# Kernel optimization log

Hardware: AMD Instinct MI355X
Metric: run time of the kernel (lower is better)

## Reference

```python
import jax, jax.numpy as jnp
import numpy as np

INPUT_DIM = 1024
OUTPUT_DIM = 1024
SPLINE_POINTS = 4

def setup_inputs() -> dict:
    key = jax.random.key(0)
    k1, k2 = jax.random.split(key)
    x = jax.random.normal(k1, (4096, INPUT_DIM), dtype=jnp.float32)
    spline_coeffs = jax.random.normal(k2, (OUTPUT_DIM, INPUT_DIM, SPLINE_POINTS, 4), dtype=jnp.float32)
    return {"x": x, "spline_coeffs": spline_coeffs}

def reference(x, spline_coeffs):
    # Per-feature min-max normalization over the batch dim (as in the torch code,
    # where x[:, j].min()/max() are taken over the batch).
    xmin = jnp.min(x, axis=0, keepdims=True)   # [1, D]
    xmax = jnp.max(x, axis=0, keepdims=True)
    xn = (x - xmin) / (xmax - xmin)            # [B, D]

    # The original sums the cubic polynomial over all spline_points, so the
    # effective coefficients are the sum over the spline_points axis.
    c = jnp.sum(spline_coeffs, axis=2)         # [O, D, 4]

    x2 = xn * xn
    x3 = x2 * xn
    # out[b, o] = sum_d c0*x^3 + c1*x^2 + c2*x + c3
    out = (jnp.einsum('bd,od->bo', x3, c[..., 0])
           + jnp.einsum('bd,od->bo', x2, c[..., 1])
           + jnp.einsum('bd,od->bo', xn, c[..., 2])
           + jnp.sum(c[..., 3], axis=1)[None, :])
    return out
```

## Files before the change

### kernel.cpp

```cpp
#include <hip/hip_runtime.h>
#include <hip/hip_bf16.h>
#include <stdint.h>
#include <stddef.h>

typedef __bf16 bf16;
typedef __attribute__((ext_vector_type(4))) __bf16 bf16x4;
typedef __attribute__((ext_vector_type(8))) __bf16 bf16x8;
typedef __attribute__((ext_vector_type(4))) float f32x4;

#define BATCH 4096
#define DIM 1024
#define ODIM 1024
#define K3 3072

#define WS_CB     0
#define WS_BIAS   6291456
#define WS_PMIN   6295552
#define WS_PMAX   7344128
#define WS_MINV   8392704
#define WS_SCALE  8396800

#define ASYNC16(g, l)                                                          \
  __builtin_amdgcn_global_load_lds(                                            \
      (__attribute__((address_space(1))) void*)(g),                            \
      (__attribute__((address_space(3))) void*)(l), 16, 0, 0)

#define BARRIER()                     \
  do {                                \
    asm volatile("" ::: "memory");    \
    __builtin_amdgcn_s_barrier();     \
    asm volatile("" ::: "memory");    \
  } while (0)
#define WAIT_VM0() __builtin_amdgcn_s_waitcnt(0x0F00 | 0x0070)
#define WAIT_LGKM() __builtin_amdgcn_s_waitcnt(0xC07F)

__global__ void k_stream(const float* __restrict__ x,
                         float* __restrict__ pmin,
                         float* __restrict__ pmax,
                         const float* __restrict__ sp,
                         bf16* __restrict__ CB,
                         float* __restrict__ bias) {
  __shared__ float red[4];
  const int t = threadIdx.x;
  if (blockIdx.x < 256) {
    const int ch = blockIdx.x;
    const float* p = x + (size_t)ch * 16 * DIM + (t << 2);
    f32x4 mn = {1e30f, 1e30f, 1e30f, 1e30f};
    f32x4 mx = {-1e30f, -1e30f, -1e30f, -1e30f};
#pragma unroll
    for (int r = 0; r < 16; ++r) {
      f32x4 v = *(const f32x4*)(p + (size_t)r * DIM);
#pragma unroll
      for (int j = 0; j < 4; ++j) {
        mn[j] = fminf(mn[j], v[j]);
        mx[j] = fmaxf(mx[j], v[j]);
      }
    }
    *(f32x4*)(pmin + ch * DIM + (t << 2)) = mn;
    *(f32x4*)(pmax + ch * DIM + (t << 2)) = mx;
  } else {
    const int o = blockIdx.x - 256;
    const int d = t << 2;
    f32x4 s[4];
#pragma unroll
    for (int dd = 0; dd < 4; ++dd) {
      const float* p = sp + ((size_t)o * DIM + d + dd) * 16;
      f32x4 acc = *(const f32x4*)(p);
      acc += *(const f32x4*)(p + 4);
      acc += *(const f32x4*)(p + 8);
      acc += *(const f32x4*)(p + 12);
      s[dd] = acc;
    }
    size_t cb = (size_t)o * K3 + d;
    bf16x4 c0 = {(bf16)s[0][0], (bf16)s[1][0], (bf16)s[2][0], (bf16)s[3][0]};
    bf16x4 c1 = {(bf16)s[0][1], (bf16)s[1][1], (bf16)s[2][1], (bf16)s[3][1]};
    bf16x4 c2 = {(bf16)s[0][2], (bf16)s[1][2], (bf16)s[2][2], (bf16)s[3][2]};
    *(bf16x4*)(CB + cb) = c0;
    *(bf16x4*)(CB + cb + 1024) = c1;
    *(bf16x4*)(CB + cb + 2048) = c2;
    float v = s[0][3] + s[1][3] + s[2][3] + s[3][3];
#pragma unroll
    for (int off = 32; off > 0; off >>= 1) v += __shfl_down(v, off, 64);
    int lane = t & 63, w = t >> 6;
    if (lane == 0) red[w] = v;
    __syncthreads();
    if (t == 0) bias[o] = red[0] + red[1] + red[2] + red[3];
  }
}

__global__ void k_minmax_final(const float* __restrict__ pmin,
                               const float* __restrict__ pmax,
                               float* __restrict__ minv,
                               float* __restrict__ scale) {
  __shared__ float smn[4][64], smx[4][64];
  const int t = threadIdx.x;
  const int lane = t & 63;
  const int w = t >> 6;
  const int col = blockIdx.x * 64 + lane;
  float mn = 1e30f, mx = -1e30f;
#pragma unroll 8
  for (int ch = w; ch < 256; ch += 4) {
    mn = fminf(mn, pmin[ch * DIM + col]);
    mx = fmaxf(mx, pmax[ch * DIM + col]);
  }
  smn[w][lane] = mn;
  smx[w][lane] = mx;
  __syncthreads();
  if (w == 0) {
    mn = fminf(fminf(smn[0][lane], smn[1][lane]), fminf(smn[2][lane], smn[3][lane]));
    mx = fmaxf(fmaxf(smx[0][lane], smx[1][lane]), fmaxf(smx[2][lane], smx[3][lane]));
    minv[col] = mn;
    scale[col] = 1.0f / (mx - mn);
  }
}

#define MSOFF 98304
#define ABUF(b) ((b) * 24576)
#define BBUF(b) (49152 + (b) * 24576)
__global__ __launch_bounds__(512, 2) void k_gemm(const float* __restrict__ x,
                                                 const float* __restrict__ minv,
                                                 const float* __restrict__ scale,
                                                 const bf16* __restrict__ CBm,
                                                 const float* __restrict__ bias,
                                                 float* __restrict__ out) {
  __shared__ __attribute__((aligned(16))) char smem[106496];

  const int tid = threadIdx.x;
  const int wave = tid >> 6;
  const int lane = tid & 63;

  const int f = blockIdx.x;
  const int chunk = f & 7;
  const int idx = f >> 3;
  const int mt = ((chunk >> 1) << 3) + (idx >> 2);
  const int nt = ((chunk & 1) << 2) + (idx & 3);
  const int bm = mt * 128;
  const int bn = nt * 128;

  const int wr = (wave >> 2) * 64;
  const int wc = (wave & 3) * 32;
  const int mrow = lane & 15;
  const int kq = lane >> 4;

  const int prow = tid >> 2;
  const int u = tid & 3;
  const int aslot = (u ^ ((prow >> 1) & 3)) << 4;
  const float* xg = x + (size_t)(bm + prow) * DIM + u * 8;

  const char* gBp = (const char*)CBm + (size_t)(bn + (tid >> 2)) * 6144 +
                    (size_t)(((tid & 3) ^ ((tid >> 3) & 3)) << 4);

  if (tid < 256) {
    f32x4 m = *(const f32x4*)(minv + tid * 4);
    *(f32x4*)(smem + MSOFF + tid * 16) = m;
  } else {
    f32x4 s = *(const f32x4*)(scale + (tid - 256) * 4);
    *(f32x4*)(smem + MSOFF + 4096 + (tid - 256) * 16) = s;
  }

  f32x4 xa, xb;
#define LOADX(dtv)                                                            \
  do {                                                                        \
    xa = *(const f32x4*)(xg + (dtv) * 32);                                    \
    xb = *(const f32x4*)(xg + (dtv) * 32 + 4);                                \
  } while (0)

#define STAGE_B(buf, dtv)                                                     \
  do {                                                                        \
    const char* gb_ = gBp + (size_t)(dtv) * 64;                               \
    char* lb_ = smem + BBUF(buf) + wave * 1024;                               \
    ASYNC16(gb_, lb_);                                                        \
    ASYNC16(gb_ + 2048, lb_ + 8192);                                          \
    ASYNC16(gb_ + 4096, lb_ + 16384);                                         \
  } while (0)

#define POWERS_WRITE(abuf, dtv)                                               \
  do {                                                                        \
    const char* msp = smem + MSOFF + ((dtv) * 32 + u * 8) * 4;                \
    f32x4 mn0 = *(const f32x4*)(msp);                                         \
    f32x4 mn1 = *(const f32x4*)(msp + 16);                                    \
    f32x4 sc0 = *(const f32x4*)(msp + 4096);                                  \
    f32x4 sc1 = *(const f32x4*)(msp + 4112);                                  \
    f32x4 n0 = (xa - mn0) * sc0, n1 = (xb - mn1) * sc1;                       \
    f32x4 q0 = n0 * n0, q1 = n1 * n1;                                         \
    f32x4 c0v = q0 * n0, c1v = q1 * n1;                                       \
    bf16x8 w1, w2, w3;                                                        \
    _Pragma("unroll") for (int e = 0; e < 4; ++e) {                           \
      w3[e] = (bf16)c0v[e]; w3[e + 4] = (bf16)c1v[e];                         \
      w2[e] = (bf16)q0[e];  w2[e + 4] = (bf16)q1[e];                          \
      w1[e] = (bf16)n0[e];  w1[e + 4] = (bf16)n1[e];                          \
    }                                                                         \
    char* aw_ = smem + ABUF(abuf) + prow * 64 + aslot;                        \
    *(bf16x8*)(aw_) = w3;                                   \
    *(bf16x8*)(aw_ + 8192) = w2;                            \
    *(bf16x8*)(aw_ + 16384) = w1;                           \
  } while (0)

  f32x4 acc[4][2] = {};

#define COMPUTE(buf)                                                          \
  do {                                                                        \
    const char* ab_ = smem + ABUF(buf);                                       \
    const char* bb_ = smem + BBUF(buf);                                       \
    _Pragma("unroll") for (int p = 0; p < 3; ++p) {                           \
      bf16x8 bg[2];                                                           \
      _Pragma("unroll") for (int j = 0; j < 2; ++j) {                         \
        int rowb = wc + j * 16 + mrow;                                        \
        bg[j] = *(const bf16x8*)(bb_ + p * 8192 + rowb * 64 +                 \
                                 ((kq ^ ((rowb >> 1) & 3)) << 4));            \
      }                                                                       \
      bf16x8 af[4];                                                           \
      _Pragma("unroll") for (int i = 0; i < 4; ++i) {                         \
        int rowa = wr + i * 16 + mrow;                                        \
        af[i] = *(const bf16x8*)(ab_ + p * 8192 + rowa * 64 +                 \
                                 ((kq ^ ((rowa >> 1) & 3)) << 4));            \
      }                                                                       \
      _Pragma("unroll") for (int i = 0; i < 4; ++i)                           \
          _Pragma("unroll") for (int j = 0; j < 2; ++j)                       \
              acc[i][j] = __builtin_amdgcn_mfma_f32_16x16x32_bf16(            \
                  af[i], bg[j], acc[i][j], 0, 0, 0);                          \
    }                                                                         \
  } while (0)

  STAGE_B(0, 0);
  LOADX(0);
  WAIT_VM0();
  WAIT_LGKM();
  BARRIER();
  POWERS_WRITE(0, 0);
  LOADX(1);
  WAIT_LGKM();
  BARRIER();

#pragma unroll 2
  for (int dt = 0; dt < 32; ++dt) {
    if (dt < 31) STAGE_B((dt + 1) & 1, dt + 1);
    COMPUTE(dt & 1);
    if (dt < 31) POWERS_WRITE((dt + 1) & 1, dt + 1);
    WAIT_VM0();
    if (dt < 30) LOADX(dt + 2);
    WAIT_LGKM();
    BARRIER();
  }

  const int ccol = lane & 15;
  const int crow = (lane >> 4) * 4;
#pragma unroll
  for (int j = 0; j < 2; ++j) {
    const int col = bn + wc + j * 16 + ccol;
    const float bv = bias[col];
#pragma unroll
    for (int i = 0; i < 4; ++i) {
      const int row0 = bm + wr + i * 16 + crow;
#pragma unroll
      for (int r = 0; r < 4; ++r)
        out[(size_t)(row0 + r) * ODIM + col] = acc[i][j][r] + bv;
    }
  }
#undef LOADX
#undef STAGE_B
#undef POWERS_WRITE
#undef COMPUTE
}

extern "C" void kernel_launch(void* const* d_in, const int* in_sizes, int n_in,
                              void* d_out, int out_size, void* d_ws, size_t ws_size,
                              hipStream_t stream) {
  (void)in_sizes; (void)n_in; (void)out_size; (void)ws_size;
  const float* x = (const float*)d_in[0];
  const float* sp = (const float*)d_in[1];
  float* out = (float*)d_out;
  char* ws = (char*)d_ws;

  bf16* CBm = (bf16*)(ws + WS_CB);
  float* bias = (float*)(ws + WS_BIAS);
  float* pmin = (float*)(ws + WS_PMIN);
  float* pmax = (float*)(ws + WS_PMAX);
  float* minv = (float*)(ws + WS_MINV);
  float* scale = (float*)(ws + WS_SCALE);

  k_stream<<<1280, 256, 0, stream>>>(x, pmin, pmax, sp, CBm, bias);
  k_minmax_final<<<16, 256, 0, stream>>>(pmin, pmax, minv, scale);
  k_gemm<<<256, 512, 0, stream>>>(x, minv, scale, CBm, bias, out);
}
```

Before: 151.1 us.

## Warp-specialize GEMM into producer/consumer waves and fuse min/max via atomics

Per-feature min/max is now reduced with order-preserving integer atomicMin in the stream kernel, which removes the second reduction kernel and its partial-min/max buffers (a memset is added instead). The GEMM is split into four producer waves and four consumer waves. Producers load x, compute the normalized powers and stage B asynchronously, while consumers only run MFMAs, each now owning a 64x64 output tile. This is meant to overlap the power computation with matrix math and drop one launch, at the cost of only half the waves doing MFMA work and atomic contention on the min/max arrays.

```diff
diff --git a/kernel.cpp b/kernel.cpp
--- a/kernel.cpp
+++ b/kernel.cpp
@@ -15,10 +15,8 @@
 
 #define WS_CB     0
 #define WS_BIAS   6291456
-#define WS_PMIN   6295552
-#define WS_PMAX   7344128
-#define WS_MINV   8392704
-#define WS_SCALE  8396800
+#define WS_UMIN   6295552
+#define WS_UMAXC  6299648
 
 #define ASYNC16(g, l)                                                          \
   __builtin_amdgcn_global_load_lds(                                            \
@@ -31,12 +29,21 @@
     __builtin_amdgcn_s_barrier();     \
     asm volatile("" ::: "memory");    \
   } while (0)
+#define WAIT_VM(n) __builtin_amdgcn_s_waitcnt(0x0F00 | 0x0070 | ((n)&15) | ((((n)>>4)&3)<<14))
 #define WAIT_VM0() __builtin_amdgcn_s_waitcnt(0x0F00 | 0x0070)
 #define WAIT_LGKM() __builtin_amdgcn_s_waitcnt(0xC07F)
 
+__device__ __forceinline__ uint32_t enc_f32(float f) {
+  uint32_t u = __float_as_uint(f);
+  return (u & 0x80000000u) ? ~u : (u | 0x80000000u);
+}
+__device__ __forceinline__ float dec_f32(uint32_t k) {
+  return __uint_as_float((k & 0x80000000u) ? (k ^ 0x80000000u) : ~k);
+}
+
 __global__ void k_stream(const float* __restrict__ x,
-                         float* __restrict__ pmin,
-                         float* __restrict__ pmax,
+                         uint32_t* __restrict__ umin,
+                         uint32_t* __restrict__ umaxc,
                          const float* __restrict__ sp,
                          bf16* __restrict__ CB,
                          float* __restrict__ bias) {
@@ -56,8 +63,12 @@
         mx[j] = fmaxf(mx[j], v[j]);
       }
     }
-    *(f32x4*)(pmin + ch * DIM + (t << 2)) = mn;
-    *(f32x4*)(pmax + ch * DIM + (t << 2)) = mx;
+    const int c = t << 2;
+#pragma unroll
+    for (int j = 0; j < 4; ++j) {
+      atomicMin(&umin[c + j], enc_f32(mn[j]));
+      atomicMin(&umaxc[c + j], ~enc_f32(mx[j]));
+    }
   } else {
     const int o = blockIdx.x - 256;
     const int d = t << 2;
@@ -88,38 +99,12 @@
   }
 }
 
-__global__ void k_minmax_final(const float* __restrict__ pmin,
-                               const float* __restrict__ pmax,
-                               float* __restrict__ minv,
-                               float* __restrict__ scale) {
-  __shared__ float smn[4][64], smx[4][64];
-  const int t = threadIdx.x;
-  const int lane = t & 63;
-  const int w = t >> 6;
-  const int col = blockIdx.x * 64 + lane;
-  float mn = 1e30f, mx = -1e30f;
-#pragma unroll 8
-  for (int ch = w; ch < 256; ch += 4) {
-    mn = fminf(mn, pmin[ch * DIM + col]);
-    mx = fmaxf(mx, pmax[ch * DIM + col]);
-  }
-  smn[w][lane] = mn;
-  smx[w][lane] = mx;
-  __syncthreads();
-  if (w == 0) {
-    mn = fminf(fminf(smn[0][lane], smn[1][lane]), fminf(smn[2][lane], smn[3][lane]));
-    mx = fmaxf(fmaxf(smx[0][lane], smx[1][lane]), fmaxf(smx[2][lane], smx[3][lane]));
-    minv[col] = mn;
-    scale[col] = 1.0f / (mx - mn);
-  }
-}
-
 #define MSOFF 98304
 #define ABUF(b) ((b) * 24576)
 #define BBUF(b) (49152 + (b) * 24576)
 __global__ __launch_bounds__(512, 2) void k_gemm(const float* __restrict__ x,
-                                                 const float* __restrict__ minv,
-                                                 const float* __restrict__ scale,
+                                                 const uint32_t* __restrict__ umin,
+                                                 const uint32_t* __restrict__ umaxc,
                                                  const bf16* __restrict__ CBm,
                                                  const float* __restrict__ bias,
                                                  float* __restrict__ out) {
@@ -137,129 +122,182 @@
   const int bm = mt * 128;
   const int bn = nt * 128;
 
-  const int wr = (wave >> 2) * 64;
-  const int wc = (wave & 3) * 32;
+  const int wr = ((wave & 3) >> 1) * 64;
+  const int wc = (wave & 1) * 64;
   const int mrow = lane & 15;
   const int kq = lane >> 4;
 
-  const int prow = tid >> 2;
-  const int u = tid & 3;
-  const int aslot = (u ^ ((prow >> 1) & 3)) << 4;
-  const float* xg = x + (size_t)(bm + prow) * DIM + u * 8;
-
-  const char* gBp = (const char*)CBm + (size_t)(bn + (tid >> 2)) * 6144 +
-                    (size_t)(((tid & 3) ^ ((tid >> 3) & 3)) << 4);
-
-  if (tid < 256) {
-    f32x4 m = *(const f32x4*)(minv + tid * 4);
-    *(f32x4*)(smem + MSOFF + tid * 16) = m;
-  } else {
-    f32x4 s = *(const f32x4*)(scale + (tid - 256) * 4);
-    *(f32x4*)(smem + MSOFF + 4096 + (tid - 256) * 16) = s;
-  }
-
-  f32x4 xa, xb;
-#define LOADX(dtv)                                                            \
+  const int ptid = (tid >= 256) ? (tid - 256) : 0;
+  const int pr = ptid >> 1;
+  const int h = tid & 1;
+  const int sA0 = ((h * 2 + 0) ^ ((pr >> 1) & 3)) << 4;
+  const int sA1 = ((h * 2 + 1) ^ ((pr >> 1) & 3)) << 4;
+  const float* xg = x + (size_t)(bm + pr) * DIM + h * 16;
+
+  const char* gB[6];
+  int ldsBoff[6];
+  if (wave >= 4) {
+    const int pk = wave - 4;
+#pragma unroll
+    for (int i = 0; i < 6; ++i) {
+      int L = (pk * 6 + i) * 1024 + lane * 16;
+      int p_ = L >> 13;
+      int rem = L & 8191;
+      int row_ = rem >> 6;
+      int u_ = (rem >> 4) & 3;
+      int us = u_ ^ ((row_ >> 1) & 3);
+      gB[i] = (const char*)CBm + (size_t)(bn + row_) * 6144 + p_ * 2048 + us * 16;
+      ldsBoff[i] = (pk * 6 + i) * 1024;
+    }
+  }
+
+  f32x4 xA0, xA1, xA2, xA3, xB0, xB1, xB2, xB3;
+#define LOADX(S, dtv)                                                         \
   do {                                                                        \
-    xa = *(const f32x4*)(xg + (dtv) * 32);                                    \
-    xb = *(const f32x4*)(xg + (dtv) * 32 + 4);                                \
+    const float* xp_ = xg + (dtv) * 32;                                       \
+    S##0 = *(const f32x4*)(xp_);                                              \
+    S##1 = *(const f32x4*)(xp_ + 4);                                          \
+    S##2 = *(const f32x4*)(xp_ + 8);                                          \
+    S##3 = *(const f32x4*)(xp_ + 12);                                         \
   } while (0)
 
 #define STAGE_B(buf, dtv)                                                     \
   do {                                                                        \
-    const char* gb_ = gBp + (size_t)(dtv) * 64;                               \
-    char* lb_ = smem + BBUF(buf) + wave * 1024;                               \
-    ASYNC16(gb_, lb_);                                                        \
-    ASYNC16(gb_ + 2048, lb_ + 8192);                                          \
-    ASYNC16(gb_ + 4096, lb_ + 16384);                                         \
-  } while (0)
-
-#define POWERS_WRITE(abuf, dtv)                                               \
+    _Pragma("unroll") for (int i_ = 0; i_ < 6; ++i_)                          \
+        ASYNC16(gB[i_] + (size_t)(dtv) * 64,                                  \
+                smem + BBUF(buf) + ldsBoff[i_]);                              \
+  } while (0)
+
+#define PK8(lo, hi, dst)                                                      \
+  _Pragma("unroll") for (int e_ = 0; e_ < 4; ++e_) {                          \
+    dst[e_] = (bf16)lo[e_];                                                   \
+    dst[e_ + 4] = (bf16)hi[e_];                                               \
+  }
+
+#define POWERS(buf, dtv, S)                                                   \
   do {                                                                        \
-    const char* msp = smem + MSOFF + ((dtv) * 32 + u * 8) * 4;                \
-    f32x4 mn0 = *(const f32x4*)(msp);                                         \
-    f32x4 mn1 = *(const f32x4*)(msp + 16);                                    \
-    f32x4 sc0 = *(const f32x4*)(msp + 4096);                                  \
-    f32x4 sc1 = *(const f32x4*)(msp + 4112);                                  \
-    f32x4 n0 = (xa - mn0) * sc0, n1 = (xb - mn1) * sc1;                       \
-    f32x4 q0 = n0 * n0, q1 = n1 * n1;                                         \
-    f32x4 c0v = q0 * n0, c1v = q1 * n1;                                       \
-    bf16x8 w1, w2, w3;                                                        \
-    _Pragma("unroll") for (int e = 0; e < 4; ++e) {                           \
-      w3[e] = (bf16)c0v[e]; w3[e + 4] = (bf16)c1v[e];                         \
-      w2[e] = (bf16)q0[e];  w2[e + 4] = (bf16)q1[e];                          \
-      w1[e] = (bf16)n0[e];  w1[e + 4] = (bf16)n1[e];                          \
-    }                                                                         \
-    char* aw_ = smem + ABUF(abuf) + prow * 64 + aslot;                        \
-    *(bf16x8*)(aw_) = w3;                                   \
-    *(bf16x8*)(aw_ + 8192) = w2;                            \
-    *(bf16x8*)(aw_ + 16384) = w1;                           \
-  } while (0)
-
-  f32x4 acc[4][2] = {};
+    const char* msp = smem + MSOFF + ((dtv) * 32 + h * 16) * 4;               \
+    f32x4 n0 = (S##0 - *(const f32x4*)(msp)) * *(const f32x4*)(msp + 4096);   \
+    f32x4 n1 = (S##1 - *(const f32x4*)(msp + 16)) * *(const f32x4*)(msp + 4112); \
+    f32x4 n2 = (S##2 - *(const f32x4*)(msp + 32)) * *(const f32x4*)(msp + 4128); \
+    f32x4 n3 = (S##3 - *(const f32x4*)(msp + 48)) * *(const f32x4*)(msp + 4144); \
+    f32x4 q0 = n0 * n0, q1 = n1 * n1, q2 = n2 * n2, q3 = n3 * n3;             \
+    f32x4 c0 = q0 * n0, c1 = q1 * n1, c2 = q2 * n2, c3 = q3 * n3;             \
+    bf16x8 w3a, w3b, w2a, w2b, w1a, w1b;                                      \
+    PK8(c0, c1, w3a) PK8(c2, c3, w3b)                                         \
+    PK8(q0, q1, w2a) PK8(q2, q3, w2b)                                         \
+    PK8(n0, n1, w1a) PK8(n2, n3, w1b)                                         \
+    char* aw_ = smem + ABUF(buf) + pr * 64;                                   \
+    *(bf16x8*)(aw_ + sA0) = w3a;                                              \
+    *(bf16x8*)(aw_ + sA1) = w3b;                                              \
+    *(bf16x8*)(aw_ + 8192 + sA0) = w2a;                                       \
+    *(bf16x8*)(aw_ + 8192 + sA1) = w2b;                                       \
+    *(bf16x8*)(aw_ + 16384 + sA0) = w1a;                                      \
+    *(bf16x8*)(aw_ + 16384 + sA1) = w1b;                                      \
+  } while (0)
+
+  f32x4 acc[4][4] = {};
 
 #define COMPUTE(buf)                                                          \
   do {                                                                        \
     const char* ab_ = smem + ABUF(buf);                                       \
     const char* bb_ = smem + BBUF(buf);                                       \
     _Pragma("unroll") for (int p = 0; p < 3; ++p) {                           \
-      bf16x8 bg[2];                                                           \
-      _Pragma("unroll") for (int j = 0; j < 2; ++j) {                         \
-        int rowb = wc + j * 16 + mrow;                                        \
-        bg[j] = *(const bf16x8*)(bb_ + p * 8192 + rowb * 64 +                 \
-                                 ((kq ^ ((rowb >> 1) & 3)) << 4));            \
-      }                                                                       \
-      bf16x8 af[4];                                                           \
+      bf16x8 af[4], bg[4];                                                    \
       _Pragma("unroll") for (int i = 0; i < 4; ++i) {                         \
         int rowa = wr + i * 16 + mrow;                                        \
         af[i] = *(const bf16x8*)(ab_ + p * 8192 + rowa * 64 +                 \
                                  ((kq ^ ((rowa >> 1) & 3)) << 4));            \
+        int rowb = wc + i * 16 + mrow;                                        \
+        bg[i] = *(const bf16x8*)(bb_ + p * 8192 + rowb * 64 +                 \
+                                 ((kq ^ ((rowb >> 1) & 3)) << 4));            \
       }                                                                       \
       _Pragma("unroll") for (int i = 0; i < 4; ++i)                           \
-          _Pragma("unroll") for (int j = 0; j < 2; ++j)                       \
+          _Pragma("unroll") for (int j = 0; j < 4; ++j)                       \
               acc[i][j] = __builtin_amdgcn_mfma_f32_16x16x32_bf16(            \
                   af[i], bg[j], acc[i][j], 0, 0, 0);                          \
     }                                                                         \
   } while (0)
 
-  STAGE_B(0, 0);
-  LOADX(0);
-  WAIT_VM0();
-  WAIT_LGKM();
+  if (wave >= 4) {
+    const int c = (tid - 256) << 2;
+    f32x4 mnv, scv;
+#pragma unroll
+    for (int j = 0; j < 4; ++j) {
+      float mnf = dec_f32(umin[c + j]);
+      float mxf = dec_f32(~umaxc[c + j]);
+      mnv[j] = mnf;
+      scv[j] = 1.0f / (mxf - mnf);
+    }
+    *(f32x4*)(smem + MSOFF + c * 4) = mnv;
+    *(f32x4*)(smem + MSOFF + 4096 + c * 4) = scv;
+    STAGE_B(0, 0);
+    LOADX(xA, 0);
+    WAIT_VM0();
+    WAIT_LGKM();
+  }
   BARRIER();
-  POWERS_WRITE(0, 0);
-  LOADX(1);
-  WAIT_LGKM();
+  if (wave >= 4) {
+    POWERS(0, 0, xA);
+    LOADX(xB, 1);
+    WAIT_LGKM();
+  }
   BARRIER();
 
-#pragma unroll 2
-  for (int dt = 0; dt < 32; ++dt) {
-    if (dt < 31) STAGE_B((dt + 1) & 1, dt + 1);
-    COMPUTE(dt & 1);
-    if (dt < 31) POWERS_WRITE((dt + 1) & 1, dt + 1);
+  for (int tt = 0; tt < 15; ++tt) {
+    const int t0 = tt * 2;
+    if (wave >= 4) {
+      STAGE_B(1, t0 + 1);
+      LOADX(xA, t0 + 2);
+      POWERS(1, t0 + 1, xB);
+      WAIT_VM(4);
+      WAIT_LGKM();
+    } else {
+      COMPUTE(0);
+    }
+    BARRIER();
+    if (wave >= 4) {
+      STAGE_B(0, t0 + 2);
+      LOADX(xB, t0 + 3);
+      POWERS(0, t0 + 2, xA);
+      WAIT_VM(4);
+      WAIT_LGKM();
+    } else {
+      COMPUTE(1);
+    }
+    BARRIER();
+  }
+  if (wave >= 4) {
+    STAGE_B(1, 31);
+    POWERS(1, 31, xB);
     WAIT_VM0();
-    if (dt < 30) LOADX(dt + 2);
     WAIT_LGKM();
-    BARRIER();
-  }
-
-  const int ccol = lane & 15;
-  const int crow = (lane >> 4) * 4;
-#pragma unroll
-  for (int j = 0; j < 2; ++j) {
-    const int col = bn + wc + j * 16 + ccol;
-    const float bv = bias[col];
-#pragma unroll
-    for (int i = 0; i < 4; ++i) {
-      const int row0 = bm + wr + i * 16 + crow;
-#pragma unroll
-      for (int r = 0; r < 4; ++r)
-        out[(size_t)(row0 + r) * ODIM + col] = acc[i][j][r] + bv;
+  } else {
+    COMPUTE(0);
+  }
+  BARRIER();
+
+  if (wave < 4) {
+    COMPUTE(1);
+    const int ccol = lane & 15;
+    const int crow = (lane >> 4) * 4;
+#pragma unroll
+    for (int j = 0; j < 4; ++j) {
+      const int col = bn + wc + j * 16 + ccol;
+      const float bv = bias[col];
+#pragma unroll
+      for (int i = 0; i < 4; ++i) {
+        const int row0 = bm + wr + i * 16 + crow;
+#pragma unroll
+        for (int r = 0; r < 4; ++r)
+          out[(size_t)(row0 + r) * ODIM + col] = acc[i][j][r] + bv;
+      }
     }
   }
 #undef LOADX
 #undef STAGE_B
-#undef POWERS_WRITE
+#undef PK8
+#undef POWERS
 #undef COMPUTE
 }
 
@@ -274,12 +312,10 @@
 
   bf16* CBm = (bf16*)(ws + WS_CB);
   float* bias = (float*)(ws + WS_BIAS);
-  float* pmin = (float*)(ws + WS_PMIN);
-  float* pmax = (float*)(ws + WS_PMAX);
-  float* minv = (float*)(ws + WS_MINV);
-  float* scale = (float*)(ws + WS_SCALE);
-
-  k_stream<<<1280, 256, 0, stream>>>(x, pmin, pmax, sp, CBm, bias);
-  k_minmax_final<<<16, 256, 0, stream>>>(pmin, pmax, minv, scale);
-  k_gemm<<<256, 512, 0, stream>>>(x, minv, scale, CBm, bias, out);
-}
+  uint32_t* umin = (uint32_t*)(ws + WS_UMIN);
+  uint32_t* umaxc = (uint32_t*)(ws + WS_UMAXC);
+
+  hipMemsetAsync(ws + WS_UMIN, 0xFF, 8192, stream);
+  k_stream<<<1280, 256, 0, stream>>>(x, umin, umaxc, sp, CBm, bias);
+  k_gemm<<<256, 512, 0, stream>>>(x, umin, umaxc, CBm, bias, out);
+}
```

Result: slower. 172.2 us (+14.0%).
